# Performance work log

Hardware: AMD Instinct MI355X
Metric: run time of the kernel (lower is better)

## Reference

```python
import jax, jax.numpy as jnp
import numpy as np
import math

DIM = 512
HEADS = 8
B = 16
P = 2048
REL_MAX = 64
REL_SIZE = 2 * REL_MAX + 1
RANK = 4
ALPHA = 16.0
QBITS = 4


def simq(w, bits=QBITS):
    # symmetric linear fake-quantization (matches simulate_quantization)
    qmin = -2 ** (bits - 1)
    qmax = 2 ** (bits - 1) - 1
    m = jnp.max(jnp.abs(w))
    scale = m / qmax
    q = jnp.clip(jnp.round(w / (scale + 1e-8)), qmin, qmax) * scale
    return jnp.where(m == 0, w, q)


def lora_lin(x, W, b, A, LB):
    # F.linear with quantized weight/bias + LoRA path
    out = x @ simq(W).T + simq(b)
    return out + (x @ A.T @ LB.T) * (ALPHA / RANK)


def setup_inputs() -> dict:
    key = jax.random.key(0)
    ks = jax.random.split(key, 20)
    d2 = DIM * 2
    inp = {
        "curr_pos": 2048,
        "z_curr_ri": jax.random.normal(ks[0], (B, DIM, 2), jnp.float32),
        "z_past_ri": jax.random.normal(ks[1], (P, B, DIM, 2), jnp.float32),
        "rel_bias_ri": jax.random.normal(ks[2], (REL_SIZE, DIM, 2), jnp.float32) * 0.02,
    }
    names = ["q", "k", "v", "o"]
    for i, n in enumerate(names):
        kw, ka, kb = jax.random.split(ks[3 + i], 3)
        inp["W" + n] = jax.random.normal(kw, (d2, d2), jnp.float32) / math.sqrt(d2)
        inp["b" + n] = jnp.zeros((d2,), jnp.float32)
        inp["A" + n] = jax.random.normal(ka, (RANK, d2), jnp.float32) / math.sqrt(d2)
        inp["LB" + n] = jax.random.normal(kb, (d2, RANK), jnp.float32) * 0.01
    return inp


def reference(curr_pos, z_curr_ri, z_past_ri, rel_bias_ri,
              Wq, bq, Aq, LBq, Wk, bk, Ak, LBk,
              Wv, bv, Av, LBv, Wo, bo, Ao, LBo):
    Bsz = z_curr_ri.shape[0]
    past_len = z_past_ri.shape[0]
    dim = z_curr_ri.shape[1]
    hd = dim // HEADS

    # projections on real-view of complex inputs ([.., dim, 2] -> [.., 2*dim])
    q = lora_lin(z_curr_ri.reshape(Bsz, dim * 2), Wq, bq, Aq, LBq)
    k = lora_lin(z_past_ri.reshape(past_len, Bsz, dim * 2), Wk, bk, Ak, LBk)
    v = lora_lin(z_past_ri.reshape(past_len, Bsz, dim * 2), Wv, bv, Av, LBv)

    q = q.reshape(Bsz, HEADS, hd, 2)            # [B,H,hd,2]
    k = k.reshape(past_len, Bsz, HEADS, hd, 2)  # [P,B,H,hd,2]
    v = v.reshape(past_len, Bsz, HEADS, hd, 2)
    qr, qi = q[..., 0], q[..., 1]
    kr, ki = k[..., 0], k[..., 1]
    vr, vi = v[..., 0], v[..., 1]

    # Re(q * conj(k)) summed over head_dim -> [B,H,P]
    dot = jnp.einsum('bhd,pbhd->bhp', qr, kr) + jnp.einsum('bhd,pbhd->bhp', qi, ki)

    # relative positional bias lookup (clamped index)
    rel_d = jnp.arange(curr_pos - past_len, curr_pos)
    idx = jnp.clip(rel_d + REL_MAX, 0, rel_bias_ri.shape[0] - 1)
    rb = rel_bias_ri[idx].reshape(past_len, HEADS, hd, 2)  # [P,H,hd,2]
    rel = jnp.einsum('bhd,phd->bhp', qr, rb[..., 0]) + jnp.einsum('bhd,phd->bhp', qi, rb[..., 1])

    w = jax.nn.softmax((dot + rel) / math.sqrt(hd), axis=-1)  # [B,H,P]

    # real softmax weights applied to complex values
    out_r = jnp.einsum('bhp,pbhd->bhd', w, vr)
    out_i = jnp.einsum('bhp,pbhd->bhd', w, vi)
    out_ri = jnp.stack([out_r, out_i], axis=-1).reshape(Bsz, dim * 2)

    o = lora_lin(out_ri, Wo, bo, Ao, LBo)
    return o.reshape(Bsz, dim, 2)  # real view of complex output [B,dim]
```

## Files before the change

kernel.cpp:

```cpp
#include <hip/hip_runtime.h>
#include <math.h>

typedef _Float16 f16;
typedef _Float16 f16x8 __attribute__((ext_vector_type(8)));
typedef _Float16 f16x4 __attribute__((ext_vector_type(4)));
typedef float f32x4 __attribute__((ext_vector_type(4)));

#define NP 2048
#define M_ROWS 32768

#define OFF_ABSMAX 0u
#define OFF_TQ     256u
#define OFF_TO     512u
#define OFF_QBIAS  1024u
#define OFF_XQH    32768u
#define OFF_XQL    65536u
#define OFF_XOH    98304u
#define OFF_XOL    131072u
#define OFF_QBUF   163840u
#define OFF_ATT    229376u
#define OFF_PM     294912u
#define OFF_PL     299008u
#define OFF_PO     303104u
#define OFF_WH     1048576u
#define OFF_TK     9437184u
#define OFF_TV     9961472u
#define OFF_KV     10485760u

__device__ __forceinline__ float qint_of(float w, float scale) {
    return fminf(7.f, fmaxf(-8.f, rintf(w / (scale + 1e-8f))));
}

__device__ __forceinline__ void gload16(const void* g, void* l) {
  __builtin_amdgcn_global_load_lds((const __attribute__((address_space(1))) void*)g,
                                   (__attribute__((address_space(3))) void*)l, 16, 0, 0);
}

__global__ void __launch_bounds__(256) absmax_kernel(
    const float* __restrict__ W0, const float* __restrict__ W1,
    const float* __restrict__ W2, const float* __restrict__ W3,
    unsigned* __restrict__ absmax) {
  int mat = blockIdx.x >> 6;
  int blk = blockIdx.x & 63;
  const float* W = mat == 0 ? W0 : mat == 1 ? W1 : mat == 2 ? W2 : W3;
  int tid = blk * 256 + threadIdx.x;
  const float4* W4 = (const float4*)W;
  float m = 0.f;
  #pragma unroll
  for (int i = 0; i < 16; ++i) {
    float4 v = W4[tid + i * 16384];
    m = fmaxf(m, fmaxf(fmaxf(fabsf(v.x), fabsf(v.y)), fmaxf(fabsf(v.z), fabsf(v.w))));
  }
  #pragma unroll
  for (int k = 32; k >= 1; k >>= 1) m = fmaxf(m, __shfl_xor(m, k));
  __shared__ float sm[4];
  if ((threadIdx.x & 63) == 0) sm[threadIdx.x >> 6] = m;
  __syncthreads();
  if (threadIdx.x == 0) {
    m = fmaxf(fmaxf(sm[0], sm[1]), fmaxf(sm[2], sm[3]));
    atomicMax(&absmax[mat], __float_as_uint(m));
  }
}

__global__ void __launch_bounds__(256) bias_quant_kernel(
    const float* __restrict__ b0, const float* __restrict__ b1,
    const float* __restrict__ b2, const float* __restrict__ b3,
    float* __restrict__ qbias) {
  int mat = blockIdx.x;
  const float* bb = mat == 0 ? b0 : mat == 1 ? b1 : mat == 2 ? b2 : b3;
  int t = threadIdx.x;
  float4 v = ((const float4*)bb)[t];
  float m = fmaxf(fmaxf(fabsf(v.x), fabsf(v.y)), fmaxf(fabsf(v.z), fabsf(v.w)));
  #pragma unroll
  for (int k = 32; k >= 1; k >>= 1) m = fmaxf(m, __shfl_xor(m, k));
  __shared__ float sm[4];
  if ((t & 63) == 0) sm[t >> 6] = m;
  __syncthreads();
  float M = fmaxf(fmaxf(sm[0], sm[1]), fmaxf(sm[2], sm[3]));
  float scale = M * (1.0f / 7.0f);
  float4 q;
  q.x = (M == 0.f) ? v.x : qint_of(v.x, scale) * scale;
  q.y = (M == 0.f) ? v.y : qint_of(v.y, scale) * scale;
  q.z = (M == 0.f) ? v.z : qint_of(v.z, scale) * scale;
  q.w = (M == 0.f) ? v.w : qint_of(v.w, scale) * scale;
  ((float4*)(qbias + mat * 1024))[t] = q;
}

__global__ void __launch_bounds__(256) quantW_kernel(
    const float* __restrict__ W0, const float* __restrict__ W1,
    const float* __restrict__ W2, const float* __restrict__ W3,
    const unsigned* __restrict__ absmax, f16* __restrict__ Wh) {
  int gid = blockIdx.x * 256 + threadIdx.x;
  int mat = gid >> 18;
  int idx = gid & 262143;
  const float* W = mat == 0 ? W0 : mat == 1 ? W1 : mat == 2 ? W2 : W3;
  float scale = __uint_as_float(absmax[mat]) * (1.0f / 7.0f);
  float4 v = ((const float4*)W)[idx];
  f16x4 r;
  r[0] = (f16)qint_of(v.x, scale);
  r[1] = (f16)qint_of(v.y, scale);
  r[2] = (f16)qint_of(v.z, scale);
  r[3] = (f16)qint_of(v.w, scale);
  *(f16x4*)(Wh + (size_t)mat * 1048576 + (size_t)idx * 4) = r;
}

__global__ void __launch_bounds__(256) cvt_hilo_kernel(
    const float* __restrict__ x, f16* __restrict__ hi, f16* __restrict__ lo) {
  int i = blockIdx.x * 256 + threadIdx.x;
  float4 v = ((const float4*)x)[i];
  f16 h0 = (f16)v.x, h1 = (f16)v.y, h2 = (f16)v.z, h3 = (f16)v.w;
  f16x4 hv = {h0, h1, h2, h3};
  f16x4 lv = {(f16)(v.x - (float)h0), (f16)(v.y - (float)h1),
              (f16)(v.z - (float)h2), (f16)(v.w - (float)h3)};
  *(f16x4*)(hi + (size_t)i * 4) = hv;
  *(f16x4*)(lo + (size_t)i * 4) = lv;
}

__global__ void __launch_bounds__(256) lora_t_small_kernel(
    const float* __restrict__ x, const float* __restrict__ A, float* __restrict__ t) {
  int tt = threadIdx.x;
  int b = tt >> 4;
  int r = (tt >> 2) & 3;
  int s = tt & 3;
  const float4* xv = (const float4*)(x + b * 1024 + s * 256);
  const float4* av = (const float4*)(A + r * 1024 + s * 256);
  float acc = 0.f;
  #pragma unroll 4
  for (int i = 0; i < 64; ++i) {
    float4 a = xv[i], c = av[i];
    acc += a.x * c.x + a.y * c.y + a.z * c.z + a.w * c.w;
  }
  acc += __shfl_xor(acc, 1);
  acc += __shfl_xor(acc, 2);
  if (s == 0) t[b * 4 + r] = acc;
}

__global__ void __launch_bounds__(256) lora_t_big_kernel(
    const float* __restrict__ zp, const float* __restrict__ Ak,
    const float* __restrict__ Av, float* __restrict__ tk, float* __restrict__ tv,
    f16* __restrict__ zph, f16* __restrict__ zpl) {
  __shared__ float sA[8 * 1024];
  for (int i = 0; i < 8; ++i) {
    int f4 = threadIdx.x + i * 256;
    float4 v = (f4 < 1024) ? ((const float4*)Ak)[f4] : ((const float4*)Av)[f4 - 1024];
    ((float4*)sA)[f4] = v;
  }
  __syncthreads();
  int lane = threadIdx.x & 63, wave = threadIdx.x >> 6;
  for (int it = 0; it < 4; ++it) {
    int m = blockIdx.x * 16 + wave * 4 + it;
    const float4* xr = (const float4*)(zp + (size_t)m * 1024);
    float acc[8] = {0.f, 0.f, 0.f, 0.f, 0.f, 0.f, 0.f, 0.f};
    for (int c = lane; c < 256; c += 64) {
      float4 xv = xr[c];
      if (zph) {
        f16 h0 = (f16)xv.x, h1 = (f16)xv.y, h2 = (f16)xv.z, h3 = (f16)xv.w;
        f16x4 hv = {h0, h1, h2, h3};
        f16x4 lv = {(f16)(xv.x - (float)h0), (f16)(xv.y - (float)h1),
                    (f16)(xv.z - (float)h2), (f16)(xv.w - (float)h3)};
        *(f16x4*)(zph + (size_t)m * 1024 + c * 4) = hv;
        *(f16x4*)(zpl + (size_t)m * 1024 + c * 4) = lv;
      }
      #pragma unroll
      for (int r = 0; r < 8; ++r) {
        float4 a = ((const float4*)sA)[r * 256 + c];
        acc[r] += xv.x * a.x + xv.y * a.y + xv.z * a.z + xv.w * a.w;
      }
    }
    #pragma unroll
    for (int k = 32; k >= 1; k >>= 1) {
      #pragma unroll
      for (int r = 0; r < 8; ++r) acc[r] += __shfl_xor(acc[r], k);
    }
    if (lane == 0) {
      tk[m * 4 + 0] = acc[0]; tk[m * 4 + 1] = acc[1];
      tk[m * 4 + 2] = acc[2]; tk[m * 4 + 3] = acc[3];
      tv[m * 4 + 0] = acc[4]; tv[m * 4 + 1] = acc[5];
      tv[m * 4 + 2] = acc[6]; tv[m * 4 + 3] = acc[7];
    }
  }
}

__global__ void __launch_bounds__(256) gemv_mfma_kernel(
    const f16* __restrict__ xhi, const f16* __restrict__ xlo,
    const f16* __restrict__ Wm, const unsigned* __restrict__ absmax, int mat,
    const float* __restrict__ qb, const float* __restrict__ t,
    const float* __restrict__ LB, float* __restrict__ out) {
  int wave = threadIdx.x >> 6, lane = threadIdx.x & 63;
  int nf = blockIdx.x * 4 + wave;
  int n0 = nf * 16;
  int row = lane & 15, kq = lane >> 4;
  f32x4 acc = {0.f, 0.f, 0.f, 0.f};
  const f16* xh = xhi + row * 1024 + kq * 8;
  const f16* xl = xlo + row * 1024 + kq * 8;
  const f16* wp = Wm + (size_t)(n0 + row) * 1024 + kq * 8;
  #pragma unroll 4
  for (int k0 = 0; k0 < 1024; k0 += 32) {
    f16x8 ah = *(const f16x8*)(xh + k0);
    f16x8 al = *(const f16x8*)(xl + k0);
    f16x8 bb = *(const f16x8*)(wp + k0);
    acc = __builtin_amdgcn_mfma_f32_16x16x32_f16(ah, bb, acc, 0, 0, 0);
    acc = __builtin_amdgcn_mfma_f32_16x16x32_f16(al, bb, acc, 0, 0, 0);
  }
  float scale = __uint_as_float(absmax[mat]) * (1.0f / 7.0f);
  int col = n0 + row;
  float bias = qb[col];
  float4 lb = *(const float4*)(LB + col * 4);
  #pragma unroll
  for (int j = 0; j < 4; ++j) {
    int m = kq * 4 + j;
    float4 tvv = *(const float4*)(t + m * 4);
    out[m * 1024 + col] =
        scale * acc[j] + bias + 4.0f * (tvv.x * lb.x + tvv.y * lb.y + tvv.z * lb.z + tvv.w * lb.w);
  }
}

template <typename KVT>
__global__ void __launch_bounds__(256, 2) kv_gemm_kernel(
    const float* __restrict__ zp, const f16* __restrict__ Wh,
    const unsigned* __restrict__ absmax, const float* __restrict__ qbias,
    const float* __restrict__ tk, const float* __restrict__ tv,
    const float* __restrict__ LBk, const float* __restrict__ LBv,
    KVT* __restrict__ kout, KVT* __restrict__ vout) {
  __shared__ __align__(16) f16 sAh[128][40];
  __shared__ __align__(16) f16 sAl[128][40];
  __shared__ __align__(16) f16 sB[128][40];
  __shared__ float sT[128][4];

  int nb = blockIdx.x;
  int m0 = blockIdx.y * 128;
  bool is_v = nb >= 8;
  int n0 = (nb & 7) * 128;
  int mat = is_v ? 2 : 1;
  const f16* Wm = Wh + (size_t)mat * 1048576;
  const float* ttv = is_v ? tv : tk;
  const float* LBm = is_v ? LBv : LBk;
  const float* qb = qbias + mat * 1024;
  KVT* outp = is_v ? vout : kout;

  int tid = threadIdx.x;
  int lane = tid & 63, wave = tid >> 6;
  int wm = (wave >> 1) * 64, wn = (wave & 1) * 64;
  int row = lane & 15, kq = lane >> 4;

  f32x4 acc[4][4];
  #pragma unroll
  for (int i = 0; i < 4; ++i)
    #pragma unroll
    for (int j = 0; j < 4; ++j) acc[i][j] = (f32x4){0.f, 0.f, 0.f, 0.f};

  int sr = tid >> 1, seg = tid & 1;
  const float* asrc = zp + (size_t)(m0 + sr) * 1024 + seg * 16;
  const f16* bsrc = Wm + (size_t)(n0 + sr) * 1024 + seg * 16;

  for (int k0 = 0; k0 < 1024; k0 += 32) {
    __syncthreads();
    float xs[16];
    const float4* a4 = (const float4*)(asrc + k0);
    *(float4*)&xs[0] = a4[0];
    *(float4*)&xs[4] = a4[1];
    *(float4*)&xs[8] = a4[2];
    *(float4*)&xs[12] = a4[3];
    f16 hs[16], ls[16];
    #pragma unroll
    for (int i = 0; i < 16; ++i) {
      f16 h = (f16)xs[i];
      hs[i] = h;
      ls[i] = (f16)(xs[i] - (float)h);
    }
    *(f16x8*)&sAh[sr][seg * 16] = *(f16x8*)&hs[0];
    *(f16x8*)&sAh[sr][seg * 16 + 8] = *(f16x8*)&hs[8];
    *(f16x8*)&sAl[sr][seg * 16] = *(f16x8*)&ls[0];
    *(f16x8*)&sAl[sr][seg * 16 + 8] = *(f16x8*)&ls[8];
    const f16x8* b8 = (const f16x8*)(bsrc + k0);
    *(f16x8*)&sB[sr][seg * 16] = b8[0];
    *(f16x8*)&sB[sr][seg * 16 + 8] = b8[1];
    __syncthreads();
    f16x8 ah[4], al[4], bf[4];
    #pragma unroll
    for (int mi = 0; mi < 4; ++mi) {
      ah[mi] = *(const f16x8*)&sAh[wm + mi * 16 + row][kq * 8];
      al[mi] = *(const f16x8*)&sAl[wm + mi * 16 + row][kq * 8];
    }
    #pragma unroll
    for (int ni = 0; ni < 4; ++ni) bf[ni] = *(const f16x8*)&sB[wn + ni * 16 + row][kq * 8];
    #pragma unroll
    for (int mi = 0; mi < 4; ++mi)
      #pragma unroll
      for (int ni = 0; ni < 4; ++ni)
        acc[mi][ni] = __builtin_amdgcn_mfma_f32_16x16x32_f16(ah[mi], bf[ni], acc[mi][ni], 0, 0, 0);
    #pragma unroll
    for (int mi = 0; mi < 4; ++mi)
      #pragma unroll
      for (int ni = 0; ni < 4; ++ni)
        acc[mi][ni] = __builtin_amdgcn_mfma_f32_16x16x32_f16(al[mi], bf[ni], acc[mi][ni], 0, 0, 0);
  }
  ((float2*)sT)[tid] = ((const float2*)(ttv + (size_t)m0 * 4))[tid];
  __syncthreads();
  float scale = __uint_as_float(absmax[mat]) * (1.0f / 7.0f);
  #pragma unroll
  for (int ni = 0; ni < 4; ++ni) {
    int ncol = n0 + wn + ni * 16 + row;
    int h = ncol >> 7, d = ncol & 127;
    float4 lb = *(const float4*)(LBm + ncol * 4);
    float bias = qb[ncol];
    #pragma unroll
    for (int mi = 0; mi < 4; ++mi) {
      #pragma unroll
      for (int j = 0; j < 4; ++j) {
        int mloc = wm + mi * 16 + kq * 4 + j;
        int m = m0 + mloc;
        int p = m >> 4, b = m & 15;
        float4 t4 = *(const float4*)&sT[mloc][0];
        float val = scale * acc[mi][ni][j] + bias +
                    4.0f * (t4.x * lb.x + t4.y * lb.y + t4.z * lb.z + t4.w * lb.w);
        outp[(((size_t)(b * 8 + h)) * 2048 + p) * 128 + d] = (KVT)val;
      }
    }
  }
}

template <typename KVT>
__global__ void __launch_bounds__(256, 3) kv_gemm_fast_kernel(
    const f16* __restrict__ zph, const f16* __restrict__ zpl,
    const f16* __restrict__ Wh, const unsigned* __restrict__ absmax,
    const float* __restrict__ qbias, const float* __restrict__ tk,
    const float* __restrict__ tv, const float* __restrict__ LBk,
    const float* __restrict__ LBv, KVT* __restrict__ kout, KVT* __restrict__ vout) {
  __shared__ __align__(16) f16 sbuf[24576];
  __shared__ float sT[128][4];
  f16* sAh = sbuf;
  f16* sAl = sbuf + 8192;
  f16* sB = sbuf + 16384;
  float* tbuf = (float*)sbuf;

  int linear = blockIdx.x + (blockIdx.y << 4);
  int xcd = linear & 7;
  int slot = linear >> 3;
  int nb = slot & 15;
  int g = ((slot >> 4) << 3) + xcd;
  int m0 = g << 7;

  bool is_v = nb >= 8;
  int n0 = (nb & 7) * 128;
  int mat = is_v ? 2 : 1;
  int h = nb & 7;
  const f16* Wm = Wh + (size_t)mat * 1048576;
  const float* ttv = is_v ? tv : tk;
  const float* LBm = is_v ? LBv : LBk;
  const float* qb = qbias + mat * 1024;
  KVT* outp = is_v ? vout : kout;

  int tid = threadIdx.x;
  int lane = tid & 63, wave = tid >> 6;
  int wm = (wave >> 1) * 64, wn = (wave & 1) * 64;
  int row = lane & 15, kq = lane >> 4;

  const f16* srcAh = zph + (size_t)m0 * 1024;
  const f16* srcAl = zpl + (size_t)m0 * 1024;
  const f16* srcB = Wm + (size_t)n0 * 1024;

  int goff[4], lbase[4];
  #pragma unroll
  for (int r = 0; r < 4; ++r) {
    int L = r * 256 + tid;
    int rw = L >> 3, cc = L & 7, cs = cc ^ (rw & 7);
    goff[r] = rw * 1024 + cs * 8;
    lbase[r] = (r * 256 + (wave << 6)) * 8;
  }

  f32x4 acc[4][4];
  #pragma unroll
  for (int i = 0; i < 4; ++i)
    #pragma unroll
    for (int j = 0; j < 4; ++j) acc[i][j] = (f32x4){0.f, 0.f, 0.f, 0.f};

  for (int k0 = 0; k0 < 1024; k0 += 64) {
    __syncthreads();
    #pragma unroll
    for (int r = 0; r < 4; ++r) {
      gload16(srcAh + goff[r] + k0, sAh + lbase[r]);
      gload16(srcAl + goff[r] + k0, sAl + lbase[r]);
      gload16(srcB + goff[r] + k0, sB + lbase[r]);
    }
    __syncthreads();
    #pragma unroll
    for (int ks = 0; ks < 2; ++ks) {
      int ch = (ks * 4 + kq) ^ (row & 7);
      f16x8 ah[4], al[4], bf[4];
      #pragma unroll
      for (int mi = 0; mi < 4; ++mi) {
        int ad = (wm + mi * 16 + row) * 64 + ch * 8;
        ah[mi] = *(const f16x8*)&sAh[ad];
        al[mi] = *(const f16x8*)&sAl[ad];
      }
      #pragma unroll
      for (int ni = 0; ni < 4; ++ni)
        bf[ni] = *(const f16x8*)&sB[(wn + ni * 16 + row) * 64 + ch * 8];
      #pragma unroll
      for (int mi = 0; mi < 4; ++mi)
        #pragma unroll
        for (int ni = 0; ni < 4; ++ni)
          acc[mi][ni] = __builtin_amdgcn_mfma_f32_16x16x32_f16(ah[mi], bf[ni], acc[mi][ni], 0, 0, 0);
      #pragma unroll
      for (int mi = 0; mi < 4; ++mi)
        #pragma unroll
        for (int ni = 0; ni < 4; ++ni)
          acc[mi][ni] = __builtin_amdgcn_mfma_f32_16x16x32_f16(al[mi], bf[ni], acc[mi][ni], 0, 0, 0);
    }
  }
  ((float2*)sT)[tid] = ((const float2*)(ttv + (size_t)m0 * 4))[tid];
  __syncthreads();
  float scale = __uint_as_float(absmax[mat]) * (1.0f / 7.0f);
  float biasv[4];
  float4 lbv[4];
  #pragma unroll
  for (int ni = 0; ni < 4; ++ni) {
    int ncol = n0 + wn + ni * 16 + row;
    biasv[ni] = qb[ncol];
    lbv[ni] = *(const float4*)(LBm + ncol * 4);
  }
  int lh = lane >> 5, l5 = lane & 31;
  #pragma unroll
  for (int halfsel = 0; halfsel < 2; ++halfsel) {
    __syncthreads();
    if ((wave >> 1) == halfsel) {
      #pragma unroll
      for (int ni = 0; ni < 4; ++ni) {
        #pragma unroll
        for (int mi = 0; mi < 4; ++mi) {
          #pragma unroll
          for (int j = 0; j < 4; ++j) {
            int ml = mi * 16 + kq * 4 + j;
            float4 t4 = *(const float4*)&sT[wm + ml][0];
            tbuf[ml * 132 + wn + ni * 16 + row] =
                scale * acc[mi][ni][j] + biasv[ni] +
                4.0f * (t4.x * lbv[ni].x + t4.y * lbv[ni].y + t4.z * lbv[ni].z +
                        t4.w * lbv[ni].w);
          }
        }
      }
    }
    __syncthreads();
    #pragma unroll
    for (int it = 0; it < 8; ++it) {
      int ml = it * 8 + wave * 2 + lh;
      int m = m0 + halfsel * 64 + ml;
      int p = m >> 4, b = m & 15;
      float4 v = *(const float4*)&tbuf[ml * 132 + l5 * 4];
      KVT* dst = outp + (((size_t)(b * 8 + h)) * 2048 + p) * 128 + l5 * 4;
      if constexpr (sizeof(KVT) == 4) {
        *(float4*)dst = v;
      } else {
        f16x4 hv = {(f16)v.x, (f16)v.y, (f16)v.z, (f16)v.w};
        *(f16x4*)dst = hv;
      }
    }
  }
}

template <typename KVT>
__device__ __forceinline__ float4 ld4(const KVT* p) {
  if constexpr (sizeof(KVT) == 4) {
    return *reinterpret_cast<const float4*>(p);
  } else {
    f16x4 v = *reinterpret_cast<const f16x4*>(p);
    return make_float4((float)v[0], (float)v[1], (float)v[2], (float)v[3]);
  }
}

template <typename KVT>
__global__ void __launch_bounds__(256) attn_part_kernel(
    const float* __restrict__ qbuf, const KVT* __restrict__ kbuf,
    const KVT* __restrict__ vbuf, const float* __restrict__ rel_bias,
    const int* __restrict__ curr_pos_p, float* __restrict__ m_part,
    float* __restrict__ l_part, float* __restrict__ o_part) {
  __shared__ float sS[256];
  __shared__ float red[8];
  __shared__ float sOv[8][132];
  int bh = blockIdx.x;
  int c = blockIdx.y;
  int b = bh >> 3, h = bh & 7;
  int p0 = c * 256;
  int tid = threadIdx.x, lane = tid & 63, wave = tid >> 6;
  int j4 = lane & 31, ph = lane >> 5;
  float4 qv = *(const float4*)(qbuf + b * 1024 + h * 128 + j4 * 4);
  int off = *curr_pos_p - NP + 64;
  const KVT* kb = kbuf + ((size_t)bh * 2048 + p0) * 128;
  for (int i = 0; i < 32; ++i) {
    int pl = i * 8 + wave * 2 + ph;
    float4 kv = ld4(kb + (size_t)pl * 128 + j4 * 4);
    int idx = min(max(p0 + pl + off, 0), 128);
    float4 rb = *(const float4*)(rel_bias + idx * 1024 + h * 128 + j4 * 4);
    float a = qv.x * (kv.x + rb.x) + qv.y * (kv.y + rb.y) +
              qv.z * (kv.z + rb.z) + qv.w * (kv.w + rb.w);
    a += __shfl_xor(a, 16);
    a += __shfl_xor(a, 8);
    a += __shfl_xor(a, 4);
    a += __shfl_xor(a, 2);
    a += __shfl_xor(a, 1);
    if (j4 == 0) sS[pl] = a * 0.125f;
  }
  __syncthreads();
  float v = sS[tid];
  float mx = v;
  #pragma unroll
  for (int k = 32; k >= 1; k >>= 1) mx = fmaxf(mx, __shfl_xor(mx, k));
  if (lane == 0) red[wave] = mx;
  __syncthreads();
  mx = fmaxf(fmaxf(red[0], red[1]), fmaxf(red[2], red[3]));
  float e = expf(v - mx);
  sS[tid] = e;
  float sum = e;
  #pragma unroll
  for (int k = 32; k >= 1; k >>= 1) sum += __shfl_xor(sum, k);
  if (lane == 0) red[4 + wave] = sum;
  __syncthreads();
  float l = red[4] + red[5] + red[6] + red[7];
  int d4 = tid & 31, pg = tid >> 5;
  const KVT* vb = vbuf + ((size_t)bh * 2048 + p0 + pg * 32) * 128;
  float4 a4 = make_float4(0.f, 0.f, 0.f, 0.f);
  #pragma unroll 4
  for (int i = 0; i < 32; ++i) {
    float s = sS[pg * 32 + i];
    float4 vv = ld4(vb + (size_t)i * 128 + d4 * 4);
    a4.x += s * vv.x;
    a4.y += s * vv.y;
    a4.z += s * vv.z;
    a4.w += s * vv.w;
  }
  *(float4*)&sOv[pg][d4 * 4] = a4;
  __syncthreads();
  if (tid < 128) {
    float o = 0.f;
    #pragma unroll
    for (int gI = 0; gI < 8; ++gI) o += sOv[gI][tid];
    int pc = bh * 8 + c;
    o_part[pc * 128 + tid] = o;
    if (tid == 0) {
      m_part[pc] = mx;
      l_part[pc] = l;
    }
  }
}

__global__ void __launch_bounds__(128) attn_combine_kernel(
    const float* __restrict__ m_part, const float* __restrict__ l_part,
    const float* __restrict__ o_part, float* __restrict__ attout) {
  int bh = blockIdx.x;
  int d = threadIdx.x;
  float M = -1e30f;
  #pragma unroll
  for (int c = 0; c < 8; ++c) M = fmaxf(M, m_part[bh * 8 + c]);
  float L = 0.f, o = 0.f;
  #pragma unroll
  for (int c = 0; c < 8; ++c) {
    float w = expf(m_part[bh * 8 + c] - M);
    L += w * l_part[bh * 8 + c];
    o += w * o_part[(bh * 8 + c) * 128 + d];
  }
  int b = bh >> 3, h = bh & 7;
  attout[b * 1024 + h * 128 + d] = o / L;
}

extern "C" void kernel_launch(void* const* d_in, const int* in_sizes, int n_in,
                              void* d_out, int out_size, void* d_ws, size_t ws_size,
                              hipStream_t stream) {
  const int* curr_pos = (const int*)d_in[0];
  const float* z_curr = (const float*)d_in[1];
  const float* z_past = (const float*)d_in[2];
  const float* rel_bias = (const float*)d_in[3];
  const float* Wq = (const float*)d_in[4];
  const float* bq = (const float*)d_in[5];
  const float* Aq = (const float*)d_in[6];
  const float* LBq = (const float*)d_in[7];
  const float* Wk = (const float*)d_in[8];
  const float* bk = (const float*)d_in[9];
  const float* Ak = (const float*)d_in[10];
  const float* LBk = (const float*)d_in[11];
  const float* Wv = (const float*)d_in[12];
  const float* bv = (const float*)d_in[13];
  const float* Av = (const float*)d_in[14];
  const float* LBv = (const float*)d_in[15];
  const float* Wo = (const float*)d_in[16];
  const float* bo = (const float*)d_in[17];
  const float* Ao = (const float*)d_in[18];
  const float* LBo = (const float*)d_in[19];

  char* ws = (char*)d_ws;
  unsigned* absmax = (unsigned*)(ws + OFF_ABSMAX);
  float* t_q = (float*)(ws + OFF_TQ);
  float* t_o = (float*)(ws + OFF_TO);
  float* qbias = (float*)(ws + OFF_QBIAS);
  f16* xqh = (f16*)(ws + OFF_XQH);
  f16* xql = (f16*)(ws + OFF_XQL);
  f16* xoh = (f16*)(ws + OFF_XOH);
  f16* xol = (f16*)(ws + OFF_XOL);
  float* qbuf = (float*)(ws + OFF_QBUF);
  float* attout = (float*)(ws + OFF_ATT);
  float* pm = (float*)(ws + OFF_PM);
  float* pl = (float*)(ws + OFF_PL);
  float* po = (float*)(ws + OFF_PO);
  f16* Wh = (f16*)(ws + OFF_WH);
  float* t_k = (float*)(ws + OFF_TK);
  float* t_v = (float*)(ws + OFF_TV);
  char* kvbase = ws + OFF_KV;

  bool f32kv = ws_size >= (size_t)OFF_KV + 2ull * 134217728ull;
  size_t kvBytes1 = f32kv ? 134217728ull : 67108864ull;
  f16* zph = (f16*)(kvbase + 2 * kvBytes1);
  f16* zpl = (f16*)(kvbase + 2 * kvBytes1 + 67108864ull);
  bool fast = ws_size >= (size_t)OFF_KV + 2 * kvBytes1 + 2ull * 67108864ull;

  hipMemsetAsync(absmax, 0, 16, stream);
  absmax_kernel<<<256, 256, 0, stream>>>(Wq, Wk, Wv, Wo, absmax);
  bias_quant_kernel<<<4, 256, 0, stream>>>(bq, bk, bv, bo, qbias);
  quantW_kernel<<<4096, 256, 0, stream>>>(Wq, Wk, Wv, Wo, absmax, Wh);
  cvt_hilo_kernel<<<16, 256, 0, stream>>>(z_curr, xqh, xql);
  lora_t_small_kernel<<<1, 256, 0, stream>>>(z_curr, Aq, t_q);
  gemv_mfma_kernel<<<16, 256, 0, stream>>>(xqh, xql, Wh, absmax, 0, qbias, t_q, LBq, qbuf);
  lora_t_big_kernel<<<2048, 256, 0, stream>>>(z_past, Ak, Av, t_k, t_v,
                                              fast ? zph : nullptr, fast ? zpl : nullptr);
  if (f32kv) {
    float* kb = (float*)kvbase;
    float* vb = (float*)(kvbase + kvBytes1);
    if (fast)
      kv_gemm_fast_kernel<float><<<dim3(16, 256), 256, 0, stream>>>(
          zph, zpl, Wh, absmax, qbias, t_k, t_v, LBk, LBv, kb, vb);
    else
      kv_gemm_kernel<float><<<dim3(16, 256), 256, 0, stream>>>(
          z_past, Wh, absmax, qbias, t_k, t_v, LBk, LBv, kb, vb);
    attn_part_kernel<float><<<dim3(128, 8), 256, 0, stream>>>(
        qbuf, kb, vb, rel_bias, curr_pos, pm, pl, po);
  } else {
    f16* kb = (f16*)kvbase;
    f16* vb = (f16*)(kvbase + kvBytes1);
    if (fast)
      kv_gemm_fast_kernel<f16><<<dim3(16, 256), 256, 0, stream>>>(
          zph, zpl, Wh, absmax, qbias, t_k, t_v, LBk, LBv, kb, vb);
    else
      kv_gemm_kernel<f16><<<dim3(16, 256), 256, 0, stream>>>(
          z_past, Wh, absmax, qbias, t_k, t_v, LBk, LBv, kb, vb);
    attn_part_kernel<f16><<<dim3(128, 8), 256, 0, stream>>>(
        qbuf, kb, vb, rel_bias, curr_pos, pm, pl, po);
  }
  attn_combine_kernel<<<128, 128, 0, stream>>>(pm, pl, po, attout);
  cvt_hilo_kernel<<<16, 256, 0, stream>>>(attout, xoh, xol);
  lora_t_small_kernel<<<1, 256, 0, stream>>>(attout, Ao, t_o);
  gemv_mfma_kernel<<<16, 256, 0, stream>>>(xoh, xol, Wh + 3ull * 1048576ull, absmax, 3,
                                           qbias + 3 * 1024, t_o, LBo, (float*)d_out);
}
```

Baseline: 827.1 us.

## Store K/V in fp16 always and double-buffer the fast KV GEMM loop

```diff
diff --git a/kernel.cpp b/kernel.cpp
--- a/kernel.cpp
+++ b/kernel.cpp
@@ -215,13 +215,12 @@
   }
 }
 
-template <typename KVT>
 __global__ void __launch_bounds__(256, 2) kv_gemm_kernel(
     const float* __restrict__ zp, const f16* __restrict__ Wh,
     const unsigned* __restrict__ absmax, const float* __restrict__ qbias,
     const float* __restrict__ tk, const float* __restrict__ tv,
     const float* __restrict__ LBk, const float* __restrict__ LBv,
-    KVT* __restrict__ kout, KVT* __restrict__ vout) {
+    f16* __restrict__ kout, f16* __restrict__ vout) {
   __shared__ __align__(16) f16 sAh[128][40];
   __shared__ __align__(16) f16 sAl[128][40];
   __shared__ __align__(16) f16 sB[128][40];
@@ -236,7 +235,7 @@
   const float* ttv = is_v ? tv : tk;
   const float* LBm = is_v ? LBv : LBk;
   const float* qb = qbias + mat * 1024;
-  KVT* outp = is_v ? vout : kout;
+  f16* outp = is_v ? vout : kout;
 
   int tid = threadIdx.x;
   int lane = tid & 63, wave = tid >> 6;
@@ -314,25 +313,20 @@
         float4 t4 = *(const float4*)&sT[mloc][0];
         float val = scale * acc[mi][ni][j] + bias +
                     4.0f * (t4.x * lb.x + t4.y * lb.y + t4.z * lb.z + t4.w * lb.w);
-        outp[(((size_t)(b * 8 + h)) * 2048 + p) * 128 + d] = (KVT)val;
+        outp[(((size_t)(b * 8 + h)) * 2048 + p) * 128 + d] = (f16)val;
       }
     }
   }
 }
 
-template <typename KVT>
 __global__ void __launch_bounds__(256, 3) kv_gemm_fast_kernel(
     const f16* __restrict__ zph, const f16* __restrict__ zpl,
     const f16* __restrict__ Wh, const unsigned* __restrict__ absmax,
     const float* __restrict__ qbias, const float* __restrict__ tk,
     const float* __restrict__ tv, const float* __restrict__ LBk,
-    const float* __restrict__ LBv, KVT* __restrict__ kout, KVT* __restrict__ vout) {
+    const float* __restrict__ LBv, f16* __restrict__ kout, f16* __restrict__ vout) {
   __shared__ __align__(16) f16 sbuf[24576];
   __shared__ float sT[128][4];
-  f16* sAh = sbuf;
-  f16* sAl = sbuf + 8192;
-  f16* sB = sbuf + 16384;
-  float* tbuf = (float*)sbuf;
 
   int linear = blockIdx.x + (blockIdx.y << 4);
   int xcd = linear & 7;
@@ -349,24 +343,25 @@
   const float* ttv = is_v ? tv : tk;
   const float* LBm = is_v ? LBv : LBk;
   const float* qb = qbias + mat * 1024;
-  KVT* outp = is_v ? vout : kout;
+  f16* outp = is_v ? vout : kout;
 
   int tid = threadIdx.x;
   int lane = tid & 63, wave = tid >> 6;
   int wm = (wave >> 1) * 64, wn = (wave & 1) * 64;
   int row = lane & 15, kq = lane >> 4;
 
-  const f16* srcAh = zph + (size_t)m0 * 1024;
-  const f16* srcAl = zpl + (size_t)m0 * 1024;
-  const f16* srcB = Wm + (size_t)n0 * 1024;
-
-  int goff[4], lbase[4];
-  #pragma unroll
-  for (int r = 0; r < 4; ++r) {
+  const f16* src0 = zph + (size_t)m0 * 1024;
+  const f16* src1 = zpl + (size_t)m0 * 1024;
+  const f16* src2 = Wm + (size_t)n0 * 1024;
+
+  int goff[2], lbase[2];
+  #pragma unroll
+  for (int r = 0; r < 2; ++r) {
     int L = r * 256 + tid;
-    int rw = L >> 3, cc = L & 7, cs = cc ^ (rw & 7);
+    int rw = L >> 2, cc = L & 3;
+    int cs = cc ^ (rw & 3) ^ ((rw >> 2) & 3);
     goff[r] = rw * 1024 + cs * 8;
-    lbase[r] = (r * 256 + (wave << 6)) * 8;
+    lbase[r] = r * 2048 + wave * 512;
   }
 
   f32x4 acc[4][4];
@@ -375,40 +370,60 @@
     #pragma unroll
     for (int j = 0; j < 4; ++j) acc[i][j] = (f32x4){0.f, 0.f, 0.f, 0.f};
 
-  for (int k0 = 0; k0 < 1024; k0 += 64) {
+  int radA[4], radB[4];
+  #pragma unroll
+  for (int mi = 0; mi < 4; ++mi) {
+    int R = wm + mi * 16 + row;
+    radA[mi] = R * 32 + ((kq ^ (R & 3) ^ ((R >> 2) & 3)) << 3);
+    int Rb = wn + mi * 16 + row;
+    radB[mi] = Rb * 32 + ((kq ^ (Rb & 3) ^ ((Rb >> 2) & 3)) << 3);
+  }
+
+  #pragma unroll
+  for (int r = 0; r < 2; ++r) {
+    gload16(src0 + goff[r], sbuf + lbase[r]);
+    gload16(src1 + goff[r], sbuf + 4096 + lbase[r]);
+    gload16(src2 + goff[r], sbuf + 8192 + lbase[r]);
+  }
+  __syncthreads();
+
+  int cur = 0;
+  for (int t = 0; t < 32; ++t) {
+    if (t < 31) {
+      int nxt = (cur ^ 1) * 12288;
+      int gk = (t + 1) * 32;
+      #pragma unroll
+      for (int r = 0; r < 2; ++r) {
+        gload16(src0 + goff[r] + gk, sbuf + nxt + lbase[r]);
+        gload16(src1 + goff[r] + gk, sbuf + nxt + 4096 + lbase[r]);
+        gload16(src2 + goff[r] + gk, sbuf + nxt + 8192 + lbase[r]);
+      }
+    }
+    const f16* bAh = sbuf + cur * 12288;
+    const f16* bAl = bAh + 4096;
+    const f16* bB = bAh + 8192;
+    f16x8 ah[4], al[4], bf[4];
+    #pragma unroll
+    for (int mi = 0; mi < 4; ++mi) {
+      ah[mi] = *(const f16x8*)&bAh[radA[mi]];
+      al[mi] = *(const f16x8*)&bAl[radA[mi]];
+    }
+    #pragma unroll
+    for (int ni = 0; ni < 4; ++ni) bf[ni] = *(const f16x8*)&bB[radB[ni]];
+    #pragma unroll
+    for (int mi = 0; mi < 4; ++mi)
+      #pragma unroll
+      for (int ni = 0; ni < 4; ++ni)
+        acc[mi][ni] = __builtin_amdgcn_mfma_f32_16x16x32_f16(ah[mi], bf[ni], acc[mi][ni], 0, 0, 0);
+    #pragma unroll
+    for (int mi = 0; mi < 4; ++mi)
+      #pragma unroll
+      for (int ni = 0; ni < 4; ++ni)
+        acc[mi][ni] = __builtin_amdgcn_mfma_f32_16x16x32_f16(al[mi], bf[ni], acc[mi][ni], 0, 0, 0);
     __syncthreads();
-    #pragma unroll
-    for (int r = 0; r < 4; ++r) {
-      gload16(srcAh + goff[r] + k0, sAh + lbase[r]);
-      gload16(srcAl + goff[r] + k0, sAl + lbase[r]);
-      gload16(srcB + goff[r] + k0, sB + lbase[r]);
-    }
-    __syncthreads();
-    #pragma unroll
-    for (int ks = 0; ks < 2; ++ks) {
-      int ch = (ks * 4 + kq) ^ (row & 7);
-      f16x8 ah[4], al[4], bf[4];
-      #pragma unroll
-      for (int mi = 0; mi < 4; ++mi) {
-        int ad = (wm + mi * 16 + row) * 64 + ch * 8;
-        ah[mi] = *(const f16x8*)&sAh[ad];
-        al[mi] = *(const f16x8*)&sAl[ad];
-      }
-      #pragma unroll
-      for (int ni = 0; ni < 4; ++ni)
-        bf[ni] = *(const f16x8*)&sB[(wn + ni * 16 + row) * 64 + ch * 8];
-      #pragma unroll
-      for (int mi = 0; mi < 4; ++mi)
-        #pragma unroll
-        for (int ni = 0; ni < 4; ++ni)
-          acc[mi][ni] = __builtin_amdgcn_mfma_f32_16x16x32_f16(ah[mi], bf[ni], acc[mi][ni], 0, 0, 0);
-      #pragma unroll
-      for (int mi = 0; mi < 4; ++mi)
-        #pragma unroll
-        for (int ni = 0; ni < 4; ++ni)
-          acc[mi][ni] = __builtin_amdgcn_mfma_f32_16x16x32_f16(al[mi], bf[ni], acc[mi][ni], 0, 0, 0);
-    }
-  }
+    cur ^= 1;
+  }
+
   ((float2*)sT)[tid] = ((const float2*)(ttv + (size_t)m0 * 4))[tid];
   __syncthreads();
   float scale = __uint_as_float(absmax[mat]) * (1.0f / 7.0f);
@@ -420,6 +435,7 @@
     biasv[ni] = qb[ncol];
     lbv[ni] = *(const float4*)(LBm + ncol * 4);
   }
+  float* tbuf = (float*)sbuf;
   int lh = lane >> 5, l5 = lane & 31;
   #pragma unroll
   for (int halfsel = 0; halfsel < 2; ++halfsel) {
@@ -448,31 +464,20 @@
       int m = m0 + halfsel * 64 + ml;
       int p = m >> 4, b = m & 15;
       float4 v = *(const float4*)&tbuf[ml * 132 + l5 * 4];
-      KVT* dst = outp + (((size_t)(b * 8 + h)) * 2048 + p) * 128 + l5 * 4;
-      if constexpr (sizeof(KVT) == 4) {
-        *(float4*)dst = v;
-      } else {
-        f16x4 hv = {(f16)v.x, (f16)v.y, (f16)v.z, (f16)v.w};
-        *(f16x4*)dst = hv;
-      }
-    }
-  }
-}
-
-template <typename KVT>
-__device__ __forceinline__ float4 ld4(const KVT* p) {
-  if constexpr (sizeof(KVT) == 4) {
-    return *reinterpret_cast<const float4*>(p);
-  } else {
-    f16x4 v = *reinterpret_cast<const f16x4*>(p);
-    return make_float4((float)v[0], (float)v[1], (float)v[2], (float)v[3]);
-  }
-}
-
-template <typename KVT>
+      f16x4 hv = {(f16)v.x, (f16)v.y, (f16)v.z, (f16)v.w};
+      *(f16x4*)(outp + (((size_t)(b * 8 + h)) * 2048 + p) * 128 + l5 * 4) = hv;
+    }
+  }
+}
+
+__device__ __forceinline__ float4 ld4h(const f16* p) {
+  f16x4 v = *reinterpret_cast<const f16x4*>(p);
+  return make_float4((float)v[0], (float)v[1], (float)v[2], (float)v[3]);
+}
+
 __global__ void __launch_bounds__(256) attn_part_kernel(
-    const float* __restrict__ qbuf, const KVT* __restrict__ kbuf,
-    const KVT* __restrict__ vbuf, const float* __restrict__ rel_bias,
+    const float* __restrict__ qbuf, const f16* __restrict__ kbuf,
+    const f16* __restrict__ vbuf, const float* __restrict__ rel_bias,
     const int* __restrict__ curr_pos_p, float* __restrict__ m_part,
     float* __restrict__ l_part, float* __restrict__ o_part) {
   __shared__ float sS[256];
@@ -486,10 +491,10 @@
   int j4 = lane & 31, ph = lane >> 5;
   float4 qv = *(const float4*)(qbuf + b * 1024 + h * 128 + j4 * 4);
   int off = *curr_pos_p - NP + 64;
-  const KVT* kb = kbuf + ((size_t)bh * 2048 + p0) * 128;
+  const f16* kb = kbuf + ((size_t)bh * 2048 + p0) * 128;
   for (int i = 0; i < 32; ++i) {
     int pl = i * 8 + wave * 2 + ph;
-    float4 kv = ld4(kb + (size_t)pl * 128 + j4 * 4);
+    float4 kv = ld4h(kb + (size_t)pl * 128 + j4 * 4);
     int idx = min(max(p0 + pl + off, 0), 128);
     float4 rb = *(const float4*)(rel_bias + idx * 1024 + h * 128 + j4 * 4);
     float a = qv.x * (kv.x + rb.x) + qv.y * (kv.y + rb.y) +
@@ -518,12 +523,12 @@
   __syncthreads();
   float l = red[4] + red[5] + red[6] + red[7];
   int d4 = tid & 31, pg = tid >> 5;
-  const KVT* vb = vbuf + ((size_t)bh * 2048 + p0 + pg * 32) * 128;
+  const f16* vb = vbuf + ((size_t)bh * 2048 + p0 + pg * 32) * 128;
   float4 a4 = make_float4(0.f, 0.f, 0.f, 0.f);
   #pragma unroll 4
   for (int i = 0; i < 32; ++i) {
     float s = sS[pg * 32 + i];
-    float4 vv = ld4(vb + (size_t)i * 128 + d4 * 4);
+    float4 vv = ld4h(vb + (size_t)i * 128 + d4 * 4);
     a4.x += s * vv.x;
     a4.y += s * vv.y;
     a4.z += s * vv.z;
@@ -606,11 +611,11 @@
   float* t_v = (float*)(ws + OFF_TV);
   char* kvbase = ws + OFF_KV;
 
-  bool f32kv = ws_size >= (size_t)OFF_KV + 2ull * 134217728ull;
-  size_t kvBytes1 = f32kv ? 134217728ull : 67108864ull;
-  f16* zph = (f16*)(kvbase + 2 * kvBytes1);
-  f16* zpl = (f16*)(kvbase + 2 * kvBytes1 + 67108864ull);
-  bool fast = ws_size >= (size_t)OFF_KV + 2 * kvBytes1 + 2ull * 67108864ull;
+  f16* kb = (f16*)kvbase;
+  f16* vb = (f16*)(kvbase + 67108864ull);
+  f16* zph = (f16*)(kvbase + 2ull * 67108864ull);
+  f16* zpl = (f16*)(kvbase + 3ull * 67108864ull);
+  bool fast = ws_size >= (size_t)OFF_KV + 4ull * 67108864ull;
 
   hipMemsetAsync(absmax, 0, 16, stream);
   absmax_kernel<<<256, 256, 0, stream>>>(Wq, Wk, Wv, Wo, absmax);
@@ -621,29 +626,14 @@
   gemv_mfma_kernel<<<16, 256, 0, stream>>>(xqh, xql, Wh, absmax, 0, qbias, t_q, LBq, qbuf);
   lora_t_big_kernel<<<2048, 256, 0, stream>>>(z_past, Ak, Av, t_k, t_v,
                                               fast ? zph : nullptr, fast ? zpl : nullptr);
-  if (f32kv) {
-    float* kb = (float*)kvbase;
-    float* vb = (float*)(kvbase + kvBytes1);
-    if (fast)
-      kv_gemm_fast_kernel<float><<<dim3(16, 256), 256, 0, stream>>>(
-          zph, zpl, Wh, absmax, qbias, t_k, t_v, LBk, LBv, kb, vb);
-    else
-      kv_gemm_kernel<float><<<dim3(16, 256), 256, 0, stream>>>(
-          z_past, Wh, absmax, qbias, t_k, t_v, LBk, LBv, kb, vb);
-    attn_part_kernel<float><<<dim3(128, 8), 256, 0, stream>>>(
-        qbuf, kb, vb, rel_bias, curr_pos, pm, pl, po);
-  } else {
-    f16* kb = (f16*)kvbase;
-    f16* vb = (f16*)(kvbase + kvBytes1);
-    if (fast)
-      kv_gemm_fast_kernel<f16><<<dim3(16, 256), 256, 0, stream>>>(
-          zph, zpl, Wh, absmax, qbias, t_k, t_v, LBk, LBv, kb, vb);
-    else
-      kv_gemm_kernel<f16><<<dim3(16, 256), 256, 0, stream>>>(
-          z_past, Wh, absmax, qbias, t_k, t_v, LBk, LBv, kb, vb);
-    attn_part_kernel<f16><<<dim3(128, 8), 256, 0, stream>>>(
-        qbuf, kb, vb, rel_bias, curr_pos, pm, pl, po);
-  }
+  if (fast)
+    kv_gemm_fast_kernel<<<dim3(16, 256), 256, 0, stream>>>(
+        zph, zpl, Wh, absmax, qbias, t_k, t_v, LBk, LBv, kb, vb);
+  else
+    kv_gemm_kernel<<<dim3(16, 256), 256, 0, stream>>>(
+        z_past, Wh, absmax, qbias, t_k, t_v, LBk, LBv, kb, vb);
+  attn_part_kernel<<<dim3(128, 8), 256, 0, stream>>>(
+      qbuf, kb, vb, rel_bias, curr_pos, pm, pl, po);
   attn_combine_kernel<<<128, 128, 0, stream>>>(pm, pl, po, attout);
   cvt_hilo_kernel<<<16, 256, 0, stream>>>(attout, xoh, xol);
   lora_t_small_kernel<<<1, 256, 0, stream>>>(attout, Ao, t_o);
```

Result: no change. 823.3 us (-0.5%).
